# Kernel tuning notes

Measured on AMD Instinct MI355X. Metric: run time of the kernel, lower is better.

Reference implementation:

```python
import jax, jax.numpy as jnp
import numpy as np

D_MODEL = 1024
N_HEADS = 16
N_KV_HEADS = 4
HEAD_DIM = 64


def setup_inputs() -> dict:
    key = jax.random.key(0)
    ks = jax.random.split(key, 5)
    B, T, P = 2, 512, 8
    scale = 1.0 / np.sqrt(D_MODEL)
    return {
        "hidden_states": jax.random.normal(ks[0], (B, T, P, D_MODEL), dtype=jnp.float32),
        # weights stored [in, out] so y = x @ W (same math as nn.Linear with W^T)
        "Wq": jax.random.normal(ks[1], (D_MODEL, N_HEADS * HEAD_DIM), dtype=jnp.float32) * scale,
        "Wk": jax.random.normal(ks[2], (D_MODEL, N_KV_HEADS * HEAD_DIM), dtype=jnp.float32) * scale,
        "Wv": jax.random.normal(ks[3], (D_MODEL, N_KV_HEADS * HEAD_DIM), dtype=jnp.float32) * scale,
        "Wo": jax.random.normal(ks[4], (N_HEADS * HEAD_DIM, D_MODEL), dtype=jnp.float32) * scale,
    }


def _rope_tables(T, d):
    half = d // 2
    inv_freq = 1.0 / (10000.0 ** (jnp.arange(half, dtype=jnp.float32) / half))
    pos = jnp.arange(T, dtype=jnp.float32)
    angles = pos[:, None] * inv_freq[None, :]  # (T, half)
    return jnp.cos(angles), jnp.sin(angles)


def _apply_rope(x, cos, sin):
    # x: (B, P, T, H, d); cos/sin: (T, d/2)
    half = x.shape[-1] // 2
    x1, x2 = x[..., :half], x[..., half:]
    c = cos[None, None, :, None, :]
    s = sin[None, None, :, None, :]
    return jnp.concatenate([x1 * c - x2 * s, x1 * s + x2 * c], axis=-1)


def reference(hidden_states, Wq, Wk, Wv, Wo):
    B, T, P, _ = hidden_states.shape
    x = jnp.transpose(hidden_states, (0, 2, 1, 3))  # (B, P, T, C)
    q = (x @ Wq).reshape(B, P, T, N_HEADS, HEAD_DIM)
    k = (x @ Wk).reshape(B, P, T, N_KV_HEADS, HEAD_DIM)
    v = (x @ Wv).reshape(B, P, T, N_KV_HEADS, HEAD_DIM)

    rep = N_HEADS // N_KV_HEADS
    k = jnp.repeat(k, rep, axis=3)  # (B,P,T,H,d) interleaved like torch repeat/view
    v = jnp.repeat(v, rep, axis=3)

    cos, sin = _rope_tables(T, HEAD_DIM)
    q = _apply_rope(q, cos, sin)
    k = _apply_rope(k, cos, sin)

    # (B,P,H,T,d)
    q = jnp.transpose(q, (0, 1, 3, 2, 4))
    k = jnp.transpose(k, (0, 1, 3, 2, 4))
    v = jnp.transpose(v, (0, 1, 3, 2, 4))

    attn = jnp.einsum("bphqd,bphkd->bphqk", q, k) / jnp.sqrt(
        jnp.asarray(HEAD_DIM, q.dtype))
    attn = jax.nn.softmax(attn, axis=-1)
    out = jnp.einsum("bphqk,bphkd->bphqd", attn, v)
    out = jnp.transpose(out, (0, 1, 3, 2, 4)).reshape(B, P, T, N_HEADS * HEAD_DIM)
    out = jnp.transpose(out, (0, 2, 1, 3))  # (B, T, P, H*d)
    return out @ Wo
```

## Files before the change

### kernel.cpp

```cpp
#include <hip/hip_runtime.h>
#include <stdint.h>


typedef __attribute__((ext_vector_type(8))) short bf16x8;
typedef __attribute__((ext_vector_type(4))) float f32x4;
typedef __attribute__((ext_vector_type(16))) float f32x16;
typedef __attribute__((ext_vector_type(4))) unsigned short us4;
typedef __attribute__((ext_vector_type(8))) unsigned short us8;

static __device__ __forceinline__ unsigned short f2bf(float f) {
  unsigned u = __float_as_uint(f);
  u += 0x7fffu + ((u >> 16) & 1u);
  return (unsigned short)(u >> 16);
}

static __device__ __forceinline__ void ld_lds16(const void* g, void* l) {
  __builtin_amdgcn_global_load_lds(
      (const __attribute__((address_space(1))) void*)g,
      (__attribute__((address_space(3))) void*)l, 16, 0, 0);
}

static __device__ __forceinline__ f32x4 mfma16(bf16x8 a, bf16x8 b, f32x4 c) {
  return __builtin_amdgcn_mfma_f32_16x16x32_bf16(a, b, c, 0, 0, 0);
}
static __device__ __forceinline__ f32x16 mfma32(bf16x8 a, bf16x8 b, f32x16 c) {
  return __builtin_amdgcn_mfma_f32_32x32x16_bf16(a, b, c, 0, 0, 0);
}

__global__ __launch_bounds__(256) void conv_all(
    const float* __restrict__ hs, const float* __restrict__ Wq,
    const float* __restrict__ Wk, const float* __restrict__ Wv,
    const float* __restrict__ Wo, unsigned short* __restrict__ xb,
    unsigned short* __restrict__ wqkv, unsigned short* __restrict__ wot) {
  __shared__ float tile[64][65];
  int bid = blockIdx.x, tid = threadIdx.x;
  if (bid < 8192) {
    int gid = bid * 256 + tid;
    size_t e = (size_t)gid * 4;
    int r = (int)(e >> 10);
    int d = (int)(e & 1023);
    int b = r >> 12, p = (r >> 9) & 7, t = r & 511;
    const float4* src = (const float4*)(hs + ((((size_t)b * 512 + t) * 8 + p) << 10) + d);
    float4 v = *src;
    us4 o;
    o.x = f2bf(v.x); o.y = f2bf(v.y); o.z = f2bf(v.z); o.w = f2bf(v.w);
    *(us4*)(xb + e) = o;
    return;
  }
  int tb = bid - 8192;
  const float* W; unsigned short* Wt; int N, tc0, tn0;
  if (tb < 256)      { W = Wq; Wt = wqkv;                       N = 1024; tc0 = (tb >> 4) * 64;          tn0 = (tb & 15) * 64; }
  else if (tb < 320) { W = Wk; Wt = wqkv + (size_t)1024 * 1024; N = 256;  tc0 = ((tb - 256) >> 2) * 64;  tn0 = ((tb - 256) & 3) * 64; }
  else if (tb < 384) { W = Wv; Wt = wqkv + (size_t)1280 * 1024; N = 256;  tc0 = ((tb - 320) >> 2) * 64;  tn0 = ((tb - 320) & 3) * 64; }
  else               { W = Wo; Wt = wot;                        N = 1024; tc0 = ((tb - 384) >> 4) * 64;  tn0 = ((tb - 384) & 15) * 64; }
  int tr = tid >> 4, tc = tid & 15;
#pragma unroll
  for (int i = 0; i < 4; ++i) {
    int c = tr + i * 16;
    float4 v = *(const float4*)(W + (size_t)(tc0 + c) * N + tn0 + tc * 4);
    tile[c][tc * 4 + 0] = v.x; tile[c][tc * 4 + 1] = v.y;
    tile[c][tc * 4 + 2] = v.z; tile[c][tc * 4 + 3] = v.w;
  }
  __syncthreads();
#pragma unroll
  for (int i = 0; i < 4; ++i) {
    int n = tr + i * 16;
    us4 o;
    o.x = f2bf(tile[tc * 4 + 0][n]); o.y = f2bf(tile[tc * 4 + 1][n]);
    o.z = f2bf(tile[tc * 4 + 2][n]); o.w = f2bf(tile[tc * 4 + 3][n]);
    *(us4*)(Wt + (size_t)(tn0 + n) * 1024 + tc0 + tc * 4) = o;
  }
}

__global__ __launch_bounds__(512, 2) void gemm_qkv(
    const unsigned short* __restrict__ A, const unsigned short* __restrict__ Bt,
    unsigned short* __restrict__ qb, unsigned short* __restrict__ kb,
    unsigned short* __restrict__ vtb) {
  constexpr int K = 1024;
  constexpr int KT = K / 64;
  __shared__ __align__(16) unsigned short Sm[2][2][256 * 64];
  unsigned short* Cs = &Sm[0][0][0];

  int tid = threadIdx.x;
  int lane = tid & 63, wid = tid >> 6;
  int quad = lane >> 4, lo = lane & 15;
  int wg = (blockIdx.x & 7) * 24 + (blockIdx.x >> 3);
  int tn = wg % 6, tm = wg / 6;
  int wr = wid >> 2, wc = wid & 3;
  int srow = lane >> 3, schunk = lane & 7;
  int cg = schunk ^ srow;

  const unsigned short* pa = A + ((size_t)(tm * 256) + wid * 8 + srow) * K + cg * 8;
  const unsigned short* pb = Bt + ((size_t)(tn * 256) + wid * 8 + srow) * K + cg * 8;

  f32x4 z = {0.f, 0.f, 0.f, 0.f};
  f32x4 acc[8][4];
#pragma unroll
  for (int i = 0; i < 8; ++i)
#pragma unroll
    for (int j = 0; j < 4; ++j) acc[i][j] = z;

  auto stage = [&](int t, int p) {
#pragma unroll
    for (int i = 0; i < 4; ++i) {
      ld_lds16(pa + (size_t)i * 64 * K + t * 64,
               (char*)&Sm[p][0][0] + (wid * 8 + i * 64) * 128);
      ld_lds16(pb + (size_t)i * 64 * K + t * 64,
               (char*)&Sm[p][1][0] + (wid * 8 + i * 64) * 128);
    }
  };

  stage(0, 0);
  stage(1, 1);
  asm volatile("s_waitcnt vmcnt(8)" ::: "memory");
  asm volatile("s_barrier" ::: "memory");

  bf16x8 af[4][2], bb0[2][2], bb1[2][2];

  for (int t = 0; t < KT; ++t) {
    int p = t & 1;
    const unsigned short* As = &Sm[p][0][0];
    const unsigned short* Bs = &Sm[p][1][0];

#pragma unroll
    for (int mi = 0; mi < 4; ++mi)
#pragma unroll
      for (int kx = 0; kx < 2; ++kx) {
        int row = wr * 128 + mi * 16 + lo;
        int cgx = (quad + kx * 4) ^ (row & 7);
        af[mi][kx] = *(const bf16x8*)(As + (size_t)row * 64 + cgx * 8);
      }
#pragma unroll
    for (int ni = 0; ni < 2; ++ni)
#pragma unroll
      for (int kx = 0; kx < 2; ++kx) {
        int row = wc * 64 + ni * 16 + lo;
        int cgx = (quad + kx * 4) ^ (row & 7);
        bb0[ni][kx] = *(const bf16x8*)(Bs + (size_t)row * 64 + cgx * 8);
      }
    asm volatile("s_barrier" ::: "memory");
    __builtin_amdgcn_s_setprio(1);
#pragma unroll
    for (int kx = 0; kx < 2; ++kx)
#pragma unroll
      for (int mi = 0; mi < 4; ++mi)
#pragma unroll
        for (int ni = 0; ni < 2; ++ni)
          acc[mi][ni] = mfma16(af[mi][kx], bb0[ni][kx], acc[mi][ni]);
    __builtin_amdgcn_s_setprio(0);
    asm volatile("s_barrier" ::: "memory");

#pragma unroll
    for (int ni = 0; ni < 2; ++ni)
#pragma unroll
      for (int kx = 0; kx < 2; ++kx) {
        int row = wc * 64 + (ni + 2) * 16 + lo;
        int cgx = (quad + kx * 4) ^ (row & 7);
        bb1[ni][kx] = *(const bf16x8*)(Bs + (size_t)row * 64 + cgx * 8);
      }
    asm volatile("s_barrier" ::: "memory");
    __builtin_amdgcn_s_setprio(1);
#pragma unroll
    for (int kx = 0; kx < 2; ++kx)
#pragma unroll
      for (int mi = 0; mi < 4; ++mi)
#pragma unroll
        for (int ni = 0; ni < 2; ++ni)
          acc[mi][ni + 2] = mfma16(af[mi][kx], bb1[ni][kx], acc[mi][ni + 2]);
    __builtin_amdgcn_s_setprio(0);
    asm volatile("s_barrier" ::: "memory");

#pragma unroll
    for (int mi = 0; mi < 4; ++mi)
#pragma unroll
      for (int kx = 0; kx < 2; ++kx) {
        int row = wr * 128 + 64 + mi * 16 + lo;
        int cgx = (quad + kx * 4) ^ (row & 7);
        af[mi][kx] = *(const bf16x8*)(As + (size_t)row * 64 + cgx * 8);
      }
    asm volatile("s_barrier" ::: "memory");
    __builtin_amdgcn_s_setprio(1);
#pragma unroll
    for (int kx = 0; kx < 2; ++kx)
#pragma unroll
      for (int mi = 0; mi < 4; ++mi)
#pragma unroll
        for (int ni = 0; ni < 2; ++ni)
          acc[mi + 4][ni + 2] = mfma16(af[mi][kx], bb1[ni][kx], acc[mi + 4][ni + 2]);
    __builtin_amdgcn_s_setprio(0);
    asm volatile("s_barrier" ::: "memory");

    bool pf = (t + 2 < KT);
    if (pf) stage(t + 2, p);
    __builtin_amdgcn_s_setprio(1);
#pragma unroll
    for (int kx = 0; kx < 2; ++kx)
#pragma unroll
      for (int mi = 0; mi < 4; ++mi)
#pragma unroll
        for (int ni = 0; ni < 2; ++ni)
          acc[mi + 4][ni] = mfma16(af[mi][kx], bb0[ni][kx], acc[mi + 4][ni]);
    __builtin_amdgcn_s_setprio(0);
    if (pf) asm volatile("s_waitcnt vmcnt(8)" ::: "memory");
    else    asm volatile("s_waitcnt vmcnt(0)" ::: "memory");
    asm volatile("s_barrier" ::: "memory");
  }

  if (tn < 5) {
    float qscale = (tn < 4) ? 0.125f : 1.0f;
#pragma unroll
    for (int mi = 0; mi < 8; ++mi)
#pragma unroll
      for (int r = 0; r < 4; ++r) {
        int row = wr * 128 + mi * 16 + quad * 4 + r;
        int tpos = (tm * 256 + row) & 511;
#pragma unroll
        for (int ni = 0; ni < 2; ++ni) {
          float invf = exp2f((float)(ni * 16 + lo) * -0.41524101186092029f);
          float ang = (float)tpos * invf;
          float s, c;
          __sincosf(ang, &s, &c);
          float x1 = acc[mi][ni][r], x2 = acc[mi][ni + 2][r];
          acc[mi][ni][r]     = (x1 * c - x2 * s) * qscale;
          acc[mi][ni + 2][r] = (x1 * s + x2 * c) * qscale;
        }
      }
#pragma unroll
    for (int mi = 0; mi < 8; ++mi)
#pragma unroll
      for (int ni = 0; ni < 4; ++ni)
#pragma unroll
        for (int r = 0; r < 4; ++r) {
          int row = wr * 128 + mi * 16 + quad * 4 + r;
          int col = wc * 64 + ni * 16 + lo;
          int cs = col ^ (((row >> 2) & 3) << 3);
          Cs[row * 256 + cs] = f2bf(acc[mi][ni][r]);
        }
    __syncthreads();
    int tc = tid & 31, ro = tid >> 5;
#pragma unroll
    for (int it = 0; it < 16; ++it) {
      int row = ro + 16 * it;
      int cs = (tc * 8) ^ (((row >> 2) & 3) << 3);
      us8 v = *(const us8*)(Cs + row * 256 + cs);
      size_t grow = (size_t)(tm * 256 + row);
      if (tn < 4) *(us8*)(qb + grow * 1024 + tn * 256 + tc * 8) = v;
      else        *(us8*)(kb + grow * 256 + tc * 8) = v;
    }
  } else {
#pragma unroll
    for (int mi = 0; mi < 8; ++mi)
#pragma unroll
      for (int ni = 0; ni < 4; ++ni)
#pragma unroll
        for (int r = 0; r < 4; ++r) {
          int trow = wr * 128 + mi * 16 + quad * 4 + r;
          int col = wc * 64 + ni * 16 + lo;
          Cs[col * 256 + (trow ^ ((col & 7) << 3))] = f2bf(acc[mi][ni][r]);
        }
    __syncthreads();
    int t0 = (tid & 31) * 8, colIdx = tid >> 5;
    int bp = tm >> 1, tbase = (tm & 1) * 256;
#pragma unroll
    for (int it = 0; it < 16; ++it) {
      int col = colIdx + it * 16;
      us8 v = *(const us8*)(Cs + col * 256 + (t0 ^ ((col & 7) << 3)));
      int hh = col >> 6, dd = col & 63;
      *(us8*)(vtb + (((size_t)(bp * 4 + hh)) * 64 + dd) * 512 + tbase + t0) = v;
    }
  }
}

__global__ __launch_bounds__(512, 2) void gemm_o(
    const unsigned short* __restrict__ A, const unsigned short* __restrict__ Bt,
    float* __restrict__ out) {
  constexpr int K = 1024;
  constexpr int KT = K / 64;
  __shared__ __align__(16) unsigned short Sm[2][(128 + 256) * 64];

  int tid = threadIdx.x;
  int lane = tid & 63, wid = tid >> 6;
  int quad = lane >> 4, lo = lane & 15;
  int wg = (blockIdx.x & 7) * 32 + (blockIdx.x >> 3);
  int tn = wg & 3, tm = wg >> 2;
  int wr = wid >> 2, wc = wid & 3;
  int srow = lane >> 3, schunk = lane & 7;
  int cg = schunk ^ srow;

  const unsigned short* pa = A + ((size_t)(tm * 128) + wid * 8 + srow) * K + cg * 8;
  const unsigned short* pb = Bt + ((size_t)(tn * 256) + wid * 8 + srow) * K + cg * 8;

  f32x4 z = {0.f, 0.f, 0.f, 0.f};
  f32x4 acc[4][4];
#pragma unroll
  for (int i = 0; i < 4; ++i)
#pragma unroll
    for (int j = 0; j < 4; ++j) acc[i][j] = z;

  auto stage = [&](int t, int p) {
    unsigned short* As = &Sm[p][0];
    unsigned short* Bs = &Sm[p][128 * 64];
#pragma unroll
    for (int i = 0; i < 2; ++i)
      ld_lds16(pa + (size_t)i * 64 * K + t * 64,
               (char*)As + (wid * 8 + i * 64) * 128);
#pragma unroll
    for (int i = 0; i < 4; ++i)
      ld_lds16(pb + (size_t)i * 64 * K + t * 64,
               (char*)Bs + (wid * 8 + i * 64) * 128);
  };

  stage(0, 0);
  stage(1, 1);
  asm volatile("s_waitcnt vmcnt(6)" ::: "memory");
  asm volatile("s_barrier" ::: "memory");

  bf16x8 af[4][2], bb0[2][2], bb1[2][2];

  for (int t = 0; t < KT; ++t) {
    int p = t & 1;
    const unsigned short* As = &Sm[p][0];
    const unsigned short* Bs = &Sm[p][128 * 64];

#pragma unroll
    for (int mi = 0; mi < 4; ++mi)
#pragma unroll
      for (int kx = 0; kx < 2; ++kx) {
        int row = wr * 64 + mi * 16 + lo;
        int cgx = (quad + kx * 4) ^ (row & 7);
        af[mi][kx] = *(const bf16x8*)(As + (size_t)row * 64 + cgx * 8);
      }
#pragma unroll
    for (int ni = 0; ni < 2; ++ni)
#pragma unroll
      for (int kx = 0; kx < 2; ++kx) {
        int row = wc * 64 + ni * 16 + lo;
        int cgx = (quad + kx * 4) ^ (row & 7);
        bb0[ni][kx] = *(const bf16x8*)(Bs + (size_t)row * 64 + cgx * 8);
      }
    asm volatile("s_barrier" ::: "memory");
    __builtin_amdgcn_s_setprio(1);
#pragma unroll
    for (int kx = 0; kx < 2; ++kx)
#pragma unroll
      for (int mi = 0; mi < 4; ++mi)
#pragma unroll
        for (int ni = 0; ni < 2; ++ni)
          acc[mi][ni] = mfma16(af[mi][kx], bb0[ni][kx], acc[mi][ni]);
    __builtin_amdgcn_s_setprio(0);
    asm volatile("s_barrier" ::: "memory");

#pragma unroll
    for (int ni = 0; ni < 2; ++ni)
#pragma unroll
      for (int kx = 0; kx < 2; ++kx) {
        int row = wc * 64 + (ni + 2) * 16 + lo;
        int cgx = (quad + kx * 4) ^ (row & 7);
        bb1[ni][kx] = *(const bf16x8*)(Bs + (size_t)row * 64 + cgx * 8);
      }
    asm volatile("s_barrier" ::: "memory");
    __builtin_amdgcn_s_setprio(1);
#pragma unroll
    for (int kx = 0; kx < 2; ++kx)
#pragma unroll
      for (int mi = 0; mi < 4; ++mi)
#pragma unroll
        for (int ni = 0; ni < 2; ++ni)
          acc[mi][ni + 2] = mfma16(af[mi][kx], bb1[ni][kx], acc[mi][ni + 2]);
    __builtin_amdgcn_s_setprio(0);
    asm volatile("s_barrier" ::: "memory");

    bool pf = (t + 2 < KT);
    if (pf) {
      stage(t + 2, p);
      asm volatile("s_waitcnt vmcnt(6)" ::: "memory");
    } else {
      asm volatile("s_waitcnt vmcnt(0)" ::: "memory");
    }
    asm volatile("s_barrier" ::: "memory");
  }

#pragma unroll
  for (int mi = 0; mi < 4; ++mi) {
    for (int ni = 0; ni < 4; ++ni) {
      int col = tn * 256 + wc * 64 + ni * 16 + lo;
      for (int r = 0; r < 4; ++r) {
        int grow = tm * 128 + wr * 64 + mi * 16 + quad * 4 + r;
        int bp = grow >> 9, tt = grow & 511;
        int b = bp >> 3, pp = bp & 7;
        out[((((size_t)b * 512 + tt) * 8 + pp) << 10) + col] = acc[mi][ni][r];
      }
    }
  }
}

__global__ __launch_bounds__(512, 4) void attn(
    const unsigned short* __restrict__ qb, const unsigned short* __restrict__ kb,
    const unsigned short* __restrict__ vtb, unsigned short* __restrict__ ao) {
  __shared__ __align__(16) unsigned short Qs[256 * 64];
  __shared__ __align__(16) unsigned short Ks[2][64 * 64];
  __shared__ __align__(16) unsigned short Vs[2][64 * 64];

  int tid = threadIdx.x;
  int lane = tid & 63, wid = tid >> 6;
  int lo32 = lane & 31, hl = lane >> 5;
  int wg = (blockIdx.x & 7) * 64 + (blockIdx.x >> 3);
  int qt = wg & 1, bph = wg >> 1;
  int head = bph & 15, bp = bph >> 4;
  int kvh = head >> 2;
  int t0 = qt * 256;
  int srow = lane >> 3, schunk = lane & 7;

  const unsigned short* qg = qb + ((size_t)(bp * 512 + t0)) * 1024 + head * 64;
  const unsigned short* kg = kb + ((size_t)bp * 512) * 256 + kvh * 64;
  const unsigned short* vg = vtb + ((size_t)(bp * 4 + kvh)) * 64 * 512;

#pragma unroll
  for (int i = 0; i < 4; ++i) {
    int row = wid * 8 + i * 64 + srow;
    int cg = schunk ^ (row & 7);
    ld_lds16(qg + (size_t)row * 1024 + cg * 8, (char*)Qs + (wid * 8 + i * 64) * 128);
  }

  auto stageKV = [&](int kt, int p) {
    int row = wid * 8 + srow;
    int cg = schunk ^ (row & 7);
    ld_lds16(kg + (size_t)(kt * 64 + row) * 256 + cg * 8, (char*)&Ks[p][0] + (wid * 8) * 128);
    ld_lds16(vg + (size_t)row * 512 + kt * 64 + cg * 8, (char*)&Vs[p][0] + (wid * 8) * 128);
  };

  stageKV(0, 0);
  stageKV(1, 1);
  asm volatile("s_waitcnt vmcnt(2)" ::: "memory");
  asm volatile("s_barrier" ::: "memory");

  f32x16 z16 = {0.f};
  f32x16 o0 = z16, o1 = z16;
  float psum = 0.f;
  int qrow = wid * 32 + lo32;

  for (int kt = 0; kt < 8; ++kt) {
    int p = kt & 1;
    const unsigned short* Kp = &Ks[p][0];
    const unsigned short* Vp = &Vs[p][0];

    f32x16 st0 = z16, st1 = z16;
#pragma unroll
    for (int kkc = 0; kkc < 4; ++kkc) {
      int ch = 2 * kkc + hl;
      bf16x8 qf = *(const bf16x8*)(Qs + (size_t)qrow * 64 + ((ch ^ (qrow & 7)) * 8));
      bf16x8 kf0 = *(const bf16x8*)(Kp + (size_t)lo32 * 64 + ((ch ^ (lo32 & 7)) * 8));
      bf16x8 kf1 = *(const bf16x8*)(Kp + (size_t)(32 + lo32) * 64 + ((ch ^ (lo32 & 7)) * 8));
      st0 = mfma32(kf0, qf, st0);
      st1 = mfma32(kf1, qf, st1);
    }

#pragma unroll
    for (int t = 0; t < 2; ++t) {
      const f32x16& stv = t ? st1 : st0;
      unsigned pk[8], xpk[8];
#pragma unroll
      for (int pp = 0; pp < 8; ++pp) {
        float e0 = __expf(stv[2 * pp]);
        float e1 = __expf(stv[2 * pp + 1]);
        psum += e0 + e1;
        pk[pp] = ((__float_as_uint(e0) + 0x8000u) >> 16) |
                 ((__float_as_uint(e1) + 0x8000u) & 0xffff0000u);
      }
#pragma unroll
      for (int pp = 0; pp < 8; ++pp) xpk[pp] = (unsigned)__shfl_xor((int)pk[pp], 32);
#pragma unroll
      for (int cc = 0; cc < 2; ++cc) {
        int o = cc * 4;
        union { unsigned u[4]; bf16x8 v; } af;
        if (hl == 0) {
          af.u[0] = pk[o];      af.u[1] = pk[o + 1];
          af.u[2] = xpk[o];     af.u[3] = xpk[o + 1];
        } else {
          af.u[0] = xpk[o + 2]; af.u[1] = xpk[o + 3];
          af.u[2] = pk[o + 2];  af.u[3] = pk[o + 3];
        }
        int vch = 2 * (t * 2 + cc) + hl;
        bf16x8 v0 = *(const bf16x8*)(Vp + (size_t)lo32 * 64 + ((vch ^ (lo32 & 7)) * 8));
        bf16x8 v1 = *(const bf16x8*)(Vp + (size_t)(32 + lo32) * 64 + ((vch ^ (lo32 & 7)) * 8));
        o0 = mfma32(af.v, v0, o0);
        o1 = mfma32(af.v, v1, o1);
      }
    }

    if (kt == 7) break;
    asm volatile("s_barrier" ::: "memory");
    if (kt < 6) {
      stageKV(kt + 2, p);
      asm volatile("s_waitcnt vmcnt(2)" ::: "memory");
    } else {
      asm volatile("s_waitcnt vmcnt(0)" ::: "memory");
    }
    asm volatile("s_barrier" ::: "memory");
  }

  psum += __shfl_xor(psum, 32);
  float inv = 1.f / psum;
#pragma unroll
  for (int r = 0; r < 16; ++r) {
    int q_r = (r & 3) + 8 * (r >> 2) + 4 * hl;
    float sc = __shfl(inv, q_r);
    size_t grow = (size_t)(bp * 512 + t0 + wid * 32 + q_r);
    ao[grow * 1024 + head * 64 + lo32]      = f2bf(o0[r] * sc);
    ao[grow * 1024 + head * 64 + 32 + lo32] = f2bf(o1[r] * sc);
  }
}

extern "C" void kernel_launch(void* const* d_in, const int* in_sizes, int n_in,
                              void* d_out, int out_size, void* d_ws, size_t ws_size,
                              hipStream_t stream) {
  const float* hs = (const float*)d_in[0];
  const float* Wq = (const float*)d_in[1];
  const float* Wk = (const float*)d_in[2];
  const float* Wv = (const float*)d_in[3];
  const float* Wo = (const float*)d_in[4];
  float* out = (float*)d_out;

  unsigned short* xb   = (unsigned short*)d_ws;
  unsigned short* wqkv = xb + (size_t)8192 * 1024;
  unsigned short* wot  = wqkv + (size_t)1536 * 1024;
  unsigned short* qbuf = wot + (size_t)1024 * 1024;
  unsigned short* kbuf = qbuf + (size_t)8192 * 1024;
  unsigned short* vtb  = kbuf + (size_t)8192 * 256;
  unsigned short* ao   = xb;

  conv_all<<<8832, 256, 0, stream>>>(hs, Wq, Wk, Wv, Wo, xb, wqkv, wot);
  gemm_qkv<<<192, 512, 0, stream>>>(xb, wqkv, qbuf, kbuf, vtb);
  attn<<<512, 512, 0, stream>>>(qbuf, kbuf, vtb, ao);
  gemm_o<<<256, 512, 0, stream>>>(ao, wot, out);
}
```

Baseline: 181.9 us.

## Fuse all four stages into one persistent cooperative kernel with grid syncs

Replaces the four separate launches (convert, QKV GEMM, attention, output GEMM) with a single cooperative kernel of 256 blocks that runs each stage in turn, separated by grid-wide syncs. The goal is to remove per-launch overhead and the gaps between kernels. The cost is that every stage is now limited to 256 blocks of 512 threads with a shared LDS budget. Stages that used to launch many more blocks (the conversion pass and attention) must loop, and the grid barriers add their own cost.

```diff
diff --git a/kernel.cpp b/kernel.cpp
--- a/kernel.cpp
+++ b/kernel.cpp
@@ -1,5 +1,8 @@
 #include <hip/hip_runtime.h>
+#include <hip/hip_cooperative_groups.h>
 #include <stdint.h>
+
+namespace cg = cooperative_groups;
 
 
 typedef __attribute__((ext_vector_type(8))) short bf16x8;
@@ -27,487 +30,507 @@
   return __builtin_amdgcn_mfma_f32_32x32x16_bf16(a, b, c, 0, 0, 0);
 }
 
-__global__ __launch_bounds__(256) void conv_all(
+__global__ __launch_bounds__(512, 2) void mega(
     const float* __restrict__ hs, const float* __restrict__ Wq,
     const float* __restrict__ Wk, const float* __restrict__ Wv,
-    const float* __restrict__ Wo, unsigned short* __restrict__ xb,
-    unsigned short* __restrict__ wqkv, unsigned short* __restrict__ wot) {
-  __shared__ float tile[64][65];
+    const float* __restrict__ Wo,
+    unsigned short* __restrict__ xb, unsigned short* __restrict__ wqkv,
+    unsigned short* __restrict__ wot, unsigned short* __restrict__ qb,
+    unsigned short* __restrict__ kb, unsigned short* __restrict__ vtb,
+    float* __restrict__ out) {
+  __shared__ __align__(16) unsigned char LDSb[131072];
+  cg::grid_group grid = cg::this_grid();
   int bid = blockIdx.x, tid = threadIdx.x;
-  if (bid < 8192) {
-    int gid = bid * 256 + tid;
-    size_t e = (size_t)gid * 4;
-    int r = (int)(e >> 10);
-    int d = (int)(e & 1023);
-    int b = r >> 12, p = (r >> 9) & 7, t = r & 511;
-    const float4* src = (const float4*)(hs + ((((size_t)b * 512 + t) * 8 + p) << 10) + d);
-    float4 v = *src;
-    us4 o;
-    o.x = f2bf(v.x); o.y = f2bf(v.y); o.z = f2bf(v.z); o.w = f2bf(v.w);
-    *(us4*)(xb + e) = o;
-    return;
+
+  {
+    float (*tile)[65] = (float(*)[65])LDSb;
+    for (int i = 0; i < 3; ++i) {
+      int tb = i * 256 + bid;
+      bool act = (tb < 640) && (tid < 256);
+      const float* W = nullptr; unsigned short* Wt = nullptr;
+      int N = 0, tc0 = 0, tn0 = 0;
+      if (act) {
+        if (tb < 256)      { W = Wq; Wt = wqkv;                       N = 1024; tc0 = (tb >> 4) * 64;          tn0 = (tb & 15) * 64; }
+        else if (tb < 320) { W = Wk; Wt = wqkv + (size_t)1024 * 1024; N = 256;  tc0 = ((tb - 256) >> 2) * 64;  tn0 = ((tb - 256) & 3) * 64; }
+        else if (tb < 384) { W = Wv; Wt = wqkv + (size_t)1280 * 1024; N = 256;  tc0 = ((tb - 320) >> 2) * 64;  tn0 = ((tb - 320) & 3) * 64; }
+        else               { W = Wo; Wt = wot;                        N = 1024; tc0 = ((tb - 384) >> 4) * 64;  tn0 = ((tb - 384) & 15) * 64; }
+      }
+      int tr = tid >> 4, tc = tid & 15;
+      if (act) {
+#pragma unroll
+        for (int k = 0; k < 4; ++k) {
+          int c = tr + k * 16;
+          float4 v = *(const float4*)(W + (size_t)(tc0 + c) * N + tn0 + tc * 4);
+          tile[c][tc * 4 + 0] = v.x; tile[c][tc * 4 + 1] = v.y;
+          tile[c][tc * 4 + 2] = v.z; tile[c][tc * 4 + 3] = v.w;
+        }
+      }
+      __syncthreads();
+      if (act) {
+#pragma unroll
+        for (int k = 0; k < 4; ++k) {
+          int n = tr + k * 16;
+          us4 o;
+          o.x = f2bf(tile[tc * 4 + 0][n]); o.y = f2bf(tile[tc * 4 + 1][n]);
+          o.z = f2bf(tile[tc * 4 + 2][n]); o.w = f2bf(tile[tc * 4 + 3][n]);
+          *(us4*)(Wt + (size_t)(tn0 + n) * 1024 + tc0 + tc * 4) = o;
+        }
+      }
+      __syncthreads();
+    }
+    for (int it = 0; it < 16; ++it) {
+      int gid = it * 131072 + bid * 512 + tid;
+      size_t e = (size_t)gid * 4;
+      int r = (int)(e >> 10);
+      int d = (int)(e & 1023);
+      int b = r >> 12, p = (r >> 9) & 7, t = r & 511;
+      const float4* src = (const float4*)(hs + ((((size_t)b * 512 + t) * 8 + p) << 10) + d);
+      float4 v = *src;
+      us4 o;
+      o.x = f2bf(v.x); o.y = f2bf(v.y); o.z = f2bf(v.z); o.w = f2bf(v.w);
+      *(us4*)(xb + e) = o;
+    }
   }
-  int tb = bid - 8192;
-  const float* W; unsigned short* Wt; int N, tc0, tn0;
-  if (tb < 256)      { W = Wq; Wt = wqkv;                       N = 1024; tc0 = (tb >> 4) * 64;          tn0 = (tb & 15) * 64; }
-  else if (tb < 320) { W = Wk; Wt = wqkv + (size_t)1024 * 1024; N = 256;  tc0 = ((tb - 256) >> 2) * 64;  tn0 = ((tb - 256) & 3) * 64; }
-  else if (tb < 384) { W = Wv; Wt = wqkv + (size_t)1280 * 1024; N = 256;  tc0 = ((tb - 320) >> 2) * 64;  tn0 = ((tb - 320) & 3) * 64; }
-  else               { W = Wo; Wt = wot;                        N = 1024; tc0 = ((tb - 384) >> 4) * 64;  tn0 = ((tb - 384) & 15) * 64; }
-  int tr = tid >> 4, tc = tid & 15;
-#pragma unroll
-  for (int i = 0; i < 4; ++i) {
-    int c = tr + i * 16;
-    float4 v = *(const float4*)(W + (size_t)(tc0 + c) * N + tn0 + tc * 4);
-    tile[c][tc * 4 + 0] = v.x; tile[c][tc * 4 + 1] = v.y;
-    tile[c][tc * 4 + 2] = v.z; tile[c][tc * 4 + 3] = v.w;
-  }
-  __syncthreads();
-#pragma unroll
-  for (int i = 0; i < 4; ++i) {
-    int n = tr + i * 16;
-    us4 o;
-    o.x = f2bf(tile[tc * 4 + 0][n]); o.y = f2bf(tile[tc * 4 + 1][n]);
-    o.z = f2bf(tile[tc * 4 + 2][n]); o.w = f2bf(tile[tc * 4 + 3][n]);
-    *(us4*)(Wt + (size_t)(tn0 + n) * 1024 + tc0 + tc * 4) = o;
-  }
-}
-
-__global__ __launch_bounds__(512, 2) void gemm_qkv(
-    const unsigned short* __restrict__ A, const unsigned short* __restrict__ Bt,
-    unsigned short* __restrict__ qb, unsigned short* __restrict__ kb,
-    unsigned short* __restrict__ vtb) {
-  constexpr int K = 1024;
-  constexpr int KT = K / 64;
-  __shared__ __align__(16) unsigned short Sm[2][2][256 * 64];
-  unsigned short* Cs = &Sm[0][0][0];
-
-  int tid = threadIdx.x;
-  int lane = tid & 63, wid = tid >> 6;
-  int quad = lane >> 4, lo = lane & 15;
-  int wg = (blockIdx.x & 7) * 24 + (blockIdx.x >> 3);
-  int tn = wg % 6, tm = wg / 6;
-  int wr = wid >> 2, wc = wid & 3;
-  int srow = lane >> 3, schunk = lane & 7;
-  int cg = schunk ^ srow;
-
-  const unsigned short* pa = A + ((size_t)(tm * 256) + wid * 8 + srow) * K + cg * 8;
-  const unsigned short* pb = Bt + ((size_t)(tn * 256) + wid * 8 + srow) * K + cg * 8;
-
-  f32x4 z = {0.f, 0.f, 0.f, 0.f};
-  f32x4 acc[8][4];
-#pragma unroll
-  for (int i = 0; i < 8; ++i)
-#pragma unroll
-    for (int j = 0; j < 4; ++j) acc[i][j] = z;
-
-  auto stage = [&](int t, int p) {
-#pragma unroll
-    for (int i = 0; i < 4; ++i) {
-      ld_lds16(pa + (size_t)i * 64 * K + t * 64,
-               (char*)&Sm[p][0][0] + (wid * 8 + i * 64) * 128);
-      ld_lds16(pb + (size_t)i * 64 * K + t * 64,
-               (char*)&Sm[p][1][0] + (wid * 8 + i * 64) * 128);
-    }
-  };
-
-  stage(0, 0);
-  stage(1, 1);
-  asm volatile("s_waitcnt vmcnt(8)" ::: "memory");
-  asm volatile("s_barrier" ::: "memory");
-
-  bf16x8 af[4][2], bb0[2][2], bb1[2][2];
-
-  for (int t = 0; t < KT; ++t) {
-    int p = t & 1;
-    const unsigned short* As = &Sm[p][0][0];
-    const unsigned short* Bs = &Sm[p][1][0];
-
-#pragma unroll
-    for (int mi = 0; mi < 4; ++mi)
-#pragma unroll
-      for (int kx = 0; kx < 2; ++kx) {
-        int row = wr * 128 + mi * 16 + lo;
-        int cgx = (quad + kx * 4) ^ (row & 7);
-        af[mi][kx] = *(const bf16x8*)(As + (size_t)row * 64 + cgx * 8);
-      }
-#pragma unroll
-    for (int ni = 0; ni < 2; ++ni)
-#pragma unroll
-      for (int kx = 0; kx < 2; ++kx) {
-        int row = wc * 64 + ni * 16 + lo;
-        int cgx = (quad + kx * 4) ^ (row & 7);
-        bb0[ni][kx] = *(const bf16x8*)(Bs + (size_t)row * 64 + cgx * 8);
-      }
+  grid.sync();
+
+  if (bid < 192) {
+    constexpr int K = 1024;
+    constexpr int KT = K / 64;
+    unsigned short* SmB = (unsigned short*)LDSb;
+    unsigned short* Cs = SmB;
+
+    int lane = tid & 63, wid = tid >> 6;
+    int quad = lane >> 4, lo = lane & 15;
+    int wg = (bid & 7) * 24 + (bid >> 3);
+    int tn = wg % 6, tm = wg / 6;
+    int wr = wid >> 2, wc = wid & 3;
+    int srow = lane >> 3, schunk = lane & 7;
+    int cg_ = schunk ^ srow;
+
+    const unsigned short* pa = xb + ((size_t)(tm * 256) + wid * 8 + srow) * K + cg_ * 8;
+    const unsigned short* pb = wqkv + ((size_t)(tn * 256) + wid * 8 + srow) * K + cg_ * 8;
+
+    f32x4 z = {0.f, 0.f, 0.f, 0.f};
+    f32x4 acc[8][4];
+#pragma unroll
+    for (int i = 0; i < 8; ++i)
+#pragma unroll
+      for (int j = 0; j < 4; ++j) acc[i][j] = z;
+
+    auto stage = [&](int t, int p) {
+#pragma unroll
+      for (int i = 0; i < 4; ++i) {
+        ld_lds16(pa + (size_t)i * 64 * K + t * 64,
+                 (char*)(SmB + (size_t)p * 2 * 16384) + (wid * 8 + i * 64) * 128);
+        ld_lds16(pb + (size_t)i * 64 * K + t * 64,
+                 (char*)(SmB + (size_t)(p * 2 + 1) * 16384) + (wid * 8 + i * 64) * 128);
+      }
+    };
+
+    stage(0, 0);
+    stage(1, 1);
+    asm volatile("s_waitcnt vmcnt(8)" ::: "memory");
     asm volatile("s_barrier" ::: "memory");
-    __builtin_amdgcn_s_setprio(1);
-#pragma unroll
-    for (int kx = 0; kx < 2; ++kx)
+
+    bf16x8 af[4][2], bb0[2][2], bb1[2][2];
+
+    for (int t = 0; t < KT; ++t) {
+      int p = t & 1;
+      const unsigned short* As = SmB + (size_t)p * 2 * 16384;
+      const unsigned short* Bs = SmB + (size_t)(p * 2 + 1) * 16384;
+
 #pragma unroll
       for (int mi = 0; mi < 4; ++mi)
 #pragma unroll
-        for (int ni = 0; ni < 2; ++ni)
-          acc[mi][ni] = mfma16(af[mi][kx], bb0[ni][kx], acc[mi][ni]);
-    __builtin_amdgcn_s_setprio(0);
-    asm volatile("s_barrier" ::: "memory");
-
-#pragma unroll
-    for (int ni = 0; ni < 2; ++ni)
-#pragma unroll
-      for (int kx = 0; kx < 2; ++kx) {
-        int row = wc * 64 + (ni + 2) * 16 + lo;
-        int cgx = (quad + kx * 4) ^ (row & 7);
-        bb1[ni][kx] = *(const bf16x8*)(Bs + (size_t)row * 64 + cgx * 8);
-      }
-    asm volatile("s_barrier" ::: "memory");
-    __builtin_amdgcn_s_setprio(1);
-#pragma unroll
-    for (int kx = 0; kx < 2; ++kx)
+        for (int kx = 0; kx < 2; ++kx) {
+          int row = wr * 128 + mi * 16 + lo;
+          int cgx = (quad + kx * 4) ^ (row & 7);
+          af[mi][kx] = *(const bf16x8*)(As + (size_t)row * 64 + cgx * 8);
+        }
+#pragma unroll
+      for (int ni = 0; ni < 2; ++ni)
+#pragma unroll
+        for (int kx = 0; kx < 2; ++kx) {
+          int row = wc * 64 + ni * 16 + lo;
+          int cgx = (quad + kx * 4) ^ (row & 7);
+          bb0[ni][kx] = *(const bf16x8*)(Bs + (size_t)row * 64 + cgx * 8);
+        }
+      asm volatile("s_barrier" ::: "memory");
+      __builtin_amdgcn_s_setprio(1);
+#pragma unroll
+      for (int kx = 0; kx < 2; ++kx)
+#pragma unroll
+        for (int mi = 0; mi < 4; ++mi)
+#pragma unroll
+          for (int ni = 0; ni < 2; ++ni)
+            acc[mi][ni] = mfma16(af[mi][kx], bb0[ni][kx], acc[mi][ni]);
+      __builtin_amdgcn_s_setprio(0);
+      asm volatile("s_barrier" ::: "memory");
+
+#pragma unroll
+      for (int ni = 0; ni < 2; ++ni)
+#pragma unroll
+        for (int kx = 0; kx < 2; ++kx) {
+          int row = wc * 64 + (ni + 2) * 16 + lo;
+          int cgx = (quad + kx * 4) ^ (row & 7);
+          bb1[ni][kx] = *(const bf16x8*)(Bs + (size_t)row * 64 + cgx * 8);
+        }
+      asm volatile("s_barrier" ::: "memory");
+      __builtin_amdgcn_s_setprio(1);
+#pragma unroll
+      for (int kx = 0; kx < 2; ++kx)
+#pragma unroll
+        for (int mi = 0; mi < 4; ++mi)
+#pragma unroll
+          for (int ni = 0; ni < 2; ++ni)
+            acc[mi][ni + 2] = mfma16(af[mi][kx], bb1[ni][kx], acc[mi][ni + 2]);
+      __builtin_amdgcn_s_setprio(0);
+      asm volatile("s_barrier" ::: "memory");
+
 #pragma unroll
       for (int mi = 0; mi < 4; ++mi)
 #pragma unroll
-        for (int ni = 0; ni < 2; ++ni)
-          acc[mi][ni + 2] = mfma16(af[mi][kx], bb1[ni][kx], acc[mi][ni + 2]);
-    __builtin_amdgcn_s_setprio(0);
-    asm volatile("s_barrier" ::: "memory");
-
-#pragma unroll
-    for (int mi = 0; mi < 4; ++mi)
-#pragma unroll
-      for (int kx = 0; kx < 2; ++kx) {
-        int row = wr * 128 + 64 + mi * 16 + lo;
-        int cgx = (quad + kx * 4) ^ (row & 7);
-        af[mi][kx] = *(const bf16x8*)(As + (size_t)row * 64 + cgx * 8);
-      }
-    asm volatile("s_barrier" ::: "memory");
-    __builtin_amdgcn_s_setprio(1);
-#pragma unroll
-    for (int kx = 0; kx < 2; ++kx)
-#pragma unroll
-      for (int mi = 0; mi < 4; ++mi)
-#pragma unroll
-        for (int ni = 0; ni < 2; ++ni)
-          acc[mi + 4][ni + 2] = mfma16(af[mi][kx], bb1[ni][kx], acc[mi + 4][ni + 2]);
-    __builtin_amdgcn_s_setprio(0);
-    asm volatile("s_barrier" ::: "memory");
-
-    bool pf = (t + 2 < KT);
-    if (pf) stage(t + 2, p);
-    __builtin_amdgcn_s_setprio(1);
-#pragma unroll
-    for (int kx = 0; kx < 2; ++kx)
-#pragma unroll
-      for (int mi = 0; mi < 4; ++mi)
-#pragma unroll
-        for (int ni = 0; ni < 2; ++ni)
-          acc[mi + 4][ni] = mfma16(af[mi][kx], bb0[ni][kx], acc[mi + 4][ni]);
-    __builtin_amdgcn_s_setprio(0);
-    if (pf) asm volatile("s_waitcnt vmcnt(8)" ::: "memory");
-    else    asm volatile("s_waitcnt vmcnt(0)" ::: "memory");
-    asm volatile("s_barrier" ::: "memory");
-  }
-
-  if (tn < 5) {
-    float qscale = (tn < 4) ? 0.125f : 1.0f;
-#pragma unroll
-    for (int mi = 0; mi < 8; ++mi)
-#pragma unroll
-      for (int r = 0; r < 4; ++r) {
-        int row = wr * 128 + mi * 16 + quad * 4 + r;
-        int tpos = (tm * 256 + row) & 511;
-#pragma unroll
-        for (int ni = 0; ni < 2; ++ni) {
-          float invf = exp2f((float)(ni * 16 + lo) * -0.41524101186092029f);
-          float ang = (float)tpos * invf;
-          float s, c;
-          __sincosf(ang, &s, &c);
-          float x1 = acc[mi][ni][r], x2 = acc[mi][ni + 2][r];
-          acc[mi][ni][r]     = (x1 * c - x2 * s) * qscale;
-          acc[mi][ni + 2][r] = (x1 * s + x2 * c) * qscale;
-        }
-      }
-#pragma unroll
-    for (int mi = 0; mi < 8; ++mi)
-#pragma unroll
-      for (int ni = 0; ni < 4; ++ni)
+        for (int kx = 0; kx < 2; ++kx) {
+          int row = wr * 128 + 64 + mi * 16 + lo;
+          int cgx = (quad + kx * 4) ^ (row & 7);
+          af[mi][kx] = *(const bf16x8*)(As + (size_t)row * 64 + cgx * 8);
+        }
+      asm volatile("s_barrier" ::: "memory");
+      __builtin_amdgcn_s_setprio(1);
+#pragma unroll
+      for (int kx = 0; kx < 2; ++kx)
+#pragma unroll
+        for (int mi = 0; mi < 4; ++mi)
+#pragma unroll
+          for (int ni = 0; ni < 2; ++ni)
+            acc[mi + 4][ni + 2] = mfma16(af[mi][kx], bb1[ni][kx], acc[mi + 4][ni + 2]);
+      __builtin_amdgcn_s_setprio(0);
+      asm volatile("s_barrier" ::: "memory");
+
+      bool pf = (t + 2 < KT);
+      if (pf) stage(t + 2, p);
+      __builtin_amdgcn_s_setprio(1);
+#pragma unroll
+      for (int kx = 0; kx < 2; ++kx)
+#pragma unroll
+        for (int mi = 0; mi < 4; ++mi)
+#pragma unroll
+          for (int ni = 0; ni < 2; ++ni)
+            acc[mi + 4][ni] = mfma16(af[mi][kx], bb0[ni][kx], acc[mi + 4][ni]);
+      __builtin_amdgcn_s_setprio(0);
+      if (pf) asm volatile("s_waitcnt vmcnt(8)" ::: "memory");
+      else    asm volatile("s_waitcnt vmcnt(0)" ::: "memory");
+      asm volatile("s_barrier" ::: "memory");
+    }
+
+    __syncthreads();
+
+    if (tn < 5) {
+      float qscale = (tn < 4) ? 0.125f : 1.0f;
+#pragma unroll
+      for (int mi = 0; mi < 8; ++mi)
 #pragma unroll
         for (int r = 0; r < 4; ++r) {
           int row = wr * 128 + mi * 16 + quad * 4 + r;
-          int col = wc * 64 + ni * 16 + lo;
-          int cs = col ^ (((row >> 2) & 3) << 3);
-          Cs[row * 256 + cs] = f2bf(acc[mi][ni][r]);
-        }
-    __syncthreads();
-    int tc = tid & 31, ro = tid >> 5;
-#pragma unroll
-    for (int it = 0; it < 16; ++it) {
-      int row = ro + 16 * it;
-      int cs = (tc * 8) ^ (((row >> 2) & 3) << 3);
-      us8 v = *(const us8*)(Cs + row * 256 + cs);
-      size_t grow = (size_t)(tm * 256 + row);
-      if (tn < 4) *(us8*)(qb + grow * 1024 + tn * 256 + tc * 8) = v;
-      else        *(us8*)(kb + grow * 256 + tc * 8) = v;
-    }
-  } else {
-#pragma unroll
-    for (int mi = 0; mi < 8; ++mi)
-#pragma unroll
-      for (int ni = 0; ni < 4; ++ni)
-#pragma unroll
+          int tpos = (tm * 256 + row) & 511;
+#pragma unroll
+          for (int ni = 0; ni < 2; ++ni) {
+            float invf = exp2f((float)(ni * 16 + lo) * -0.41524101186092029f);
+            float ang = (float)tpos * invf;
+            float s, c;
+            __sincosf(ang, &s, &c);
+            float x1 = acc[mi][ni][r], x2 = acc[mi][ni + 2][r];
+            acc[mi][ni][r]     = (x1 * c - x2 * s) * qscale;
+            acc[mi][ni + 2][r] = (x1 * s + x2 * c) * qscale;
+          }
+        }
+#pragma unroll
+      for (int mi = 0; mi < 8; ++mi)
+#pragma unroll
+        for (int ni = 0; ni < 4; ++ni)
+#pragma unroll
+          for (int r = 0; r < 4; ++r) {
+            int row = wr * 128 + mi * 16 + quad * 4 + r;
+            int col = wc * 64 + ni * 16 + lo;
+            int cs = col ^ (((row >> 2) & 3) << 3);
+            Cs[row * 256 + cs] = f2bf(acc[mi][ni][r]);
+          }
+      __syncthreads();
+      int tc = tid & 31, ro = tid >> 5;
+#pragma unroll
+      for (int it = 0; it < 16; ++it) {
+        int row = ro + 16 * it;
+        int cs = (tc * 8) ^ (((row >> 2) & 3) << 3);
+        us8 v = *(const us8*)(Cs + row * 256 + cs);
+        size_t grow = (size_t)(tm * 256 + row);
+        if (tn < 4) *(us8*)(qb + grow * 1024 + tn * 256 + tc * 8) = v;
+        else        *(us8*)(kb + grow * 256 + tc * 8) = v;
+      }
+    } else {
+#pragma unroll
+      for (int mi = 0; mi < 8; ++mi)
+#pragma unroll
+        for (int ni = 0; ni < 4; ++ni)
+#pragma unroll
+          for (int r = 0; r < 4; ++r) {
+            int trow = wr * 128 + mi * 16 + quad * 4 + r;
+            int col = wc * 64 + ni * 16 + lo;
+            Cs[col * 256 + (trow ^ ((col & 7) << 3))] = f2bf(acc[mi][ni][r]);
+          }
+      __syncthreads();
+      int t0 = (tid & 31) * 8, colIdx = tid >> 5;
+      int bp = tm >> 1, tbase = (tm & 1) * 256;
+#pragma unroll
+      for (int it = 0; it < 16; ++it) {
+        int col = colIdx + it * 16;
+        us8 v = *(const us8*)(Cs + col * 256 + (t0 ^ ((col & 7) << 3)));
+        int hh = col >> 6, dd = col & 63;
+        *(us8*)(vtb + (((size_t)(bp * 4 + hh)) * 64 + dd) * 512 + tbase + t0) = v;
+      }
+    }
+  }
+  grid.sync();
+
+  {
+    unsigned short* Qs = (unsigned short*)LDSb;
+    unsigned short* KsB = Qs + 256 * 64;
+    unsigned short* VsB = KsB + 2 * 64 * 64;
+    unsigned short* ao = xb;
+
+    int lane = tid & 63, wid = tid >> 6;
+    int lo32 = lane & 31, hl = lane >> 5;
+    int srow = lane >> 3, schunk = lane & 7;
+
+    for (int u = 0; u < 2; ++u) {
+      __syncthreads();
+      int uu = bid + u * 256;
+      int wg = (uu & 7) * 64 + (uu >> 3);
+      int qt = wg & 1, bph = wg >> 1;
+      int head = bph & 15, bp = bph >> 4;
+      int kvh = head >> 2;
+      int t0 = qt * 256;
+
+      const unsigned short* qg = qb + ((size_t)(bp * 512 + t0)) * 1024 + head * 64;
+      const unsigned short* kg = kb + ((size_t)bp * 512) * 256 + kvh * 64;
+      const unsigned short* vg = vtb + ((size_t)(bp * 4 + kvh)) * 64 * 512;
+
+#pragma unroll
+      for (int i = 0; i < 4; ++i) {
+        int row = wid * 8 + i * 64 + srow;
+        int cg_ = schunk ^ (row & 7);
+        ld_lds16(qg + (size_t)row * 1024 + cg_ * 8, (char*)Qs + (wid * 8 + i * 64) * 128);
+      }
+
+      auto stageKV = [&](int kt, int p) {
+        int row = wid * 8 + srow;
+        int cg_ = schunk ^ (row & 7);
+        ld_lds16(kg + (size_t)(kt * 64 + row) * 256 + cg_ * 8, (char*)(KsB + p * 4096) + (wid * 8) * 128);
+        ld_lds16(vg + (size_t)row * 512 + kt * 64 + cg_ * 8, (char*)(VsB + p * 4096) + (wid * 8) * 128);
+      };
+
+      stageKV(0, 0);
+      stageKV(1, 1);
+      asm volatile("s_waitcnt vmcnt(2)" ::: "memory");
+      asm volatile("s_barrier" ::: "memory");
+
+      f32x16 z16 = {0.f};
+      f32x16 o0 = z16, o1 = z16;
+      float psum = 0.f;
+      int qrow = wid * 32 + lo32;
+
+      for (int kt = 0; kt < 8; ++kt) {
+        int p = kt & 1;
+        const unsigned short* Kp = KsB + p * 4096;
+        const unsigned short* Vp = VsB + p * 4096;
+
+        f32x16 st0 = z16, st1 = z16;
+#pragma unroll
+        for (int kkc = 0; kkc < 4; ++kkc) {
+          int ch = 2 * kkc + hl;
+          bf16x8 qf = *(const bf16x8*)(Qs + (size_t)qrow * 64 + ((ch ^ (qrow & 7)) * 8));
+          bf16x8 kf0 = *(const bf16x8*)(Kp + (size_t)lo32 * 64 + ((ch ^ (lo32 & 7)) * 8));
+          bf16x8 kf1 = *(const bf16x8*)(Kp + (size_t)(32 + lo32) * 64 + ((ch ^ (lo32 & 7)) * 8));
+          st0 = mfma32(kf0, qf, st0);
+          st1 = mfma32(kf1, qf, st1);
+        }
+
+#pragma unroll
+        for (int t = 0; t < 2; ++t) {
+          const f32x16& stv = t ? st1 : st0;
+          unsigned pk[8], xpk[8];
+#pragma unroll
+          for (int pp = 0; pp < 8; ++pp) {
+            float e0 = __expf(stv[2 * pp]);
+            float e1 = __expf(stv[2 * pp + 1]);
+            psum += e0 + e1;
+            pk[pp] = ((__float_as_uint(e0) + 0x8000u) >> 16) |
+                     ((__float_as_uint(e1) + 0x8000u) & 0xffff0000u);
+          }
+#pragma unroll
+          for (int pp = 0; pp < 8; ++pp) xpk[pp] = (unsigned)__shfl_xor((int)pk[pp], 32);
+#pragma unroll
+          for (int cc = 0; cc < 2; ++cc) {
+            int o = cc * 4;
+            union { unsigned u[4]; bf16x8 v; } afr;
+            if (hl == 0) {
+              afr.u[0] = pk[o];      afr.u[1] = pk[o + 1];
+              afr.u[2] = xpk[o];     afr.u[3] = xpk[o + 1];
+            } else {
+              afr.u[0] = xpk[o + 2]; afr.u[1] = xpk[o + 3];
+              afr.u[2] = pk[o + 2];  afr.u[3] = pk[o + 3];
+            }
+            int vch = 2 * (t * 2 + cc) + hl;
+            bf16x8 v0 = *(const bf16x8*)(Vp + (size_t)lo32 * 64 + ((vch ^ (lo32 & 7)) * 8));
+            bf16x8 v1 = *(const bf16x8*)(Vp + (size_t)(32 + lo32) * 64 + ((vch ^ (lo32 & 7)) * 8));
+            o0 = mfma32(afr.v, v0, o0);
+            o1 = mfma32(afr.v, v1, o1);
+          }
+        }
+
+        if (kt == 7) break;
+        asm volatile("s_barrier" ::: "memory");
+        if (kt < 6) {
+          stageKV(kt + 2, p);
+          asm volatile("s_waitcnt vmcnt(2)" ::: "memory");
+        } else {
+          asm volatile("s_waitcnt vmcnt(0)" ::: "memory");
+        }
+        asm volatile("s_barrier" ::: "memory");
+      }
+
+      psum += __shfl_xor(psum, 32);
+      float inv = 1.f / psum;
+#pragma unroll
+      for (int r = 0; r < 16; ++r) {
+        int q_r = (r & 3) + 8 * (r >> 2) + 4 * hl;
+        float sc = __shfl(inv, q_r);
+        size_t grow = (size_t)(bp * 512 + t0 + wid * 32 + q_r);
+        ao[grow * 1024 + head * 64 + lo32]      = f2bf(o0[r] * sc);
+        ao[grow * 1024 + head * 64 + 32 + lo32] = f2bf(o1[r] * sc);
+      }
+    }
+  }
+  grid.sync();
+
+  {
+    constexpr int K = 1024;
+    constexpr int KT = K / 64;
+    unsigned short* SmD = (unsigned short*)LDSb;
+    const unsigned short* Ain = xb;
+
+    int lane = tid & 63, wid = tid >> 6;
+    int quad = lane >> 4, lo = lane & 15;
+    int wg = (bid & 7) * 32 + (bid >> 3);
+    int tn = wg & 3, tm = wg >> 2;
+    int wr = wid >> 2, wc = wid & 3;
+    int srow = lane >> 3, schunk = lane & 7;
+    int cg_ = schunk ^ srow;
+
+    const unsigned short* pa = Ain + ((size_t)(tm * 128) + wid * 8 + srow) * K + cg_ * 8;
+    const unsigned short* pb = wot + ((size_t)(tn * 256) + wid * 8 + srow) * K + cg_ * 8;
+
+    f32x4 z = {0.f, 0.f, 0.f, 0.f};
+    f32x4 acc[4][4];
+#pragma unroll
+    for (int i = 0; i < 4; ++i)
+#pragma unroll
+      for (int j = 0; j < 4; ++j) acc[i][j] = z;
+
+    auto stage = [&](int t, int p) {
+      unsigned short* As = SmD + (size_t)p * 24576;
+      unsigned short* Bs = As + 128 * 64;
+#pragma unroll
+      for (int i = 0; i < 2; ++i)
+        ld_lds16(pa + (size_t)i * 64 * K + t * 64,
+                 (char*)As + (wid * 8 + i * 64) * 128);
+#pragma unroll
+      for (int i = 0; i < 4; ++i)
+        ld_lds16(pb + (size_t)i * 64 * K + t * 64,
+                 (char*)Bs + (wid * 8 + i * 64) * 128);
+    };
+
+    stage(0, 0);
+    stage(1, 1);
+    asm volatile("s_waitcnt vmcnt(6)" ::: "memory");
+    asm volatile("s_barrier" ::: "memory");
+
+    bf16x8 af[4][2], bb0[2][2], bb1[2][2];
+
+    for (int t = 0; t < KT; ++t) {
+      int p = t & 1;
+      const unsigned short* As = SmD + (size_t)p * 24576;
+      const unsigned short* Bs = As + 128 * 64;
+
+#pragma unroll
+      for (int mi = 0; mi < 4; ++mi)
+#pragma unroll
+        for (int kx = 0; kx < 2; ++kx) {
+          int row = wr * 64 + mi * 16 + lo;
+          int cgx = (quad + kx * 4) ^ (row & 7);
+          af[mi][kx] = *(const bf16x8*)(As + (size_t)row * 64 + cgx * 8);
+        }
+#pragma unroll
+      for (int ni = 0; ni < 2; ++ni)
+#pragma unroll
+        for (int kx = 0; kx < 2; ++kx) {
+          int row = wc * 64 + ni * 16 + lo;
+          int cgx = (quad + kx * 4) ^ (row & 7);
+          bb0[ni][kx] = *(const bf16x8*)(Bs + (size_t)row * 64 + cgx * 8);
+        }
+      asm volatile("s_barrier" ::: "memory");
+      __builtin_amdgcn_s_setprio(1);
+#pragma unroll
+      for (int kx = 0; kx < 2; ++kx)
+#pragma unroll
+        for (int mi = 0; mi < 4; ++mi)
+#pragma unroll
+          for (int ni = 0; ni < 2; ++ni)
+            acc[mi][ni] = mfma16(af[mi][kx], bb0[ni][kx], acc[mi][ni]);
+      __builtin_amdgcn_s_setprio(0);
+      asm volatile("s_barrier" ::: "memory");
+
+#pragma unroll
+      for (int ni = 0; ni < 2; ++ni)
+#pragma unroll
+        for (int kx = 0; kx < 2; ++kx) {
+          int row = wc * 64 + (ni + 2) * 16 + lo;
+          int cgx = (quad + kx * 4) ^ (row & 7);
+          bb1[ni][kx] = *(const bf16x8*)(Bs + (size_t)row * 64 + cgx * 8);
+        }
+      asm volatile("s_barrier" ::: "memory");
+      __builtin_amdgcn_s_setprio(1);
+#pragma unroll
+      for (int kx = 0; kx < 2; ++kx)
+#pragma unroll
+        for (int mi = 0; mi < 4; ++mi)
+#pragma unroll
+          for (int ni = 0; ni < 2; ++ni)
+            acc[mi][ni + 2] = mfma16(af[mi][kx], bb1[ni][kx], acc[mi][ni + 2]);
+      __builtin_amdgcn_s_setprio(0);
+      asm volatile("s_barrier" ::: "memory");
+
+      bool pf = (t + 2 < KT);
+      if (pf) {
+        stage(t + 2, p);
+        asm volatile("s_waitcnt vmcnt(6)" ::: "memory");
+      } else {
+        asm volatile("s_waitcnt vmcnt(0)" ::: "memory");
+      }
+      asm volatile("s_barrier" ::: "memory");
+    }
+
+#pragma unroll
+    for (int mi = 0; mi < 4; ++mi) {
+      for (int ni = 0; ni < 4; ++ni) {
+        int col = tn * 256 + wc * 64 + ni * 16 + lo;
         for (int r = 0; r < 4; ++r) {
-          int trow = wr * 128 + mi * 16 + quad * 4 + r;
-          int col = wc * 64 + ni * 16 + lo;
-          Cs[col * 256 + (trow ^ ((col & 7) << 3))] = f2bf(acc[mi][ni][r]);
-        }
-    __syncthreads();
-    int t0 = (tid & 31) * 8, colIdx = tid >> 5;
-    int bp = tm >> 1, tbase = (tm & 1) * 256;
-#pragma unroll
-    for (int it = 0; it < 16; ++it) {
-      int col = colIdx + it * 16;
-      us8 v = *(const us8*)(Cs + col * 256 + (t0 ^ ((col & 7) << 3)));
-      int hh = col >> 6, dd = col & 63;
-      *(us8*)(vtb + (((size_t)(bp * 4 + hh)) * 64 + dd) * 512 + tbase + t0) = v;
-    }
-  }
-}
-
-__global__ __launch_bounds__(512, 2) void gemm_o(
-    const unsigned short* __restrict__ A, const unsigned short* __restrict__ Bt,
-    float* __restrict__ out) {
-  constexpr int K = 1024;
-  constexpr int KT = K / 64;
-  __shared__ __align__(16) unsigned short Sm[2][(128 + 256) * 64];
-
-  int tid = threadIdx.x;
-  int lane = tid & 63, wid = tid >> 6;
-  int quad = lane >> 4, lo = lane & 15;
-  int wg = (blockIdx.x & 7) * 32 + (blockIdx.x >> 3);
-  int tn = wg & 3, tm = wg >> 2;
-  int wr = wid >> 2, wc = wid & 3;
-  int srow = lane >> 3, schunk = lane & 7;
-  int cg = schunk ^ srow;
-
-  const unsigned short* pa = A + ((size_t)(tm * 128) + wid * 8 + srow) * K + cg * 8;
-  const unsigned short* pb = Bt + ((size_t)(tn * 256) + wid * 8 + srow) * K + cg * 8;
-
-  f32x4 z = {0.f, 0.f, 0.f, 0.f};
-  f32x4 acc[4][4];
-#pragma unroll
-  for (int i = 0; i < 4; ++i)
-#pragma unroll
-    for (int j = 0; j < 4; ++j) acc[i][j] = z;
-
-  auto stage = [&](int t, int p) {
-    unsigned short* As = &Sm[p][0];
-    unsigned short* Bs = &Sm[p][128 * 64];
-#pragma unroll
-    for (int i = 0; i < 2; ++i)
-      ld_lds16(pa + (size_t)i * 64 * K + t * 64,
-               (char*)As + (wid * 8 + i * 64) * 128);
-#pragma unroll
-    for (int i = 0; i < 4; ++i)
-      ld_lds16(pb + (size_t)i * 64 * K + t * 64,
-               (char*)Bs + (wid * 8 + i * 64) * 128);
-  };
-
-  stage(0, 0);
-  stage(1, 1);
-  asm volatile("s_waitcnt vmcnt(6)" ::: "memory");
-  asm volatile("s_barrier" ::: "memory");
-
-  bf16x8 af[4][2], bb0[2][2], bb1[2][2];
-
-  for (int t = 0; t < KT; ++t) {
-    int p = t & 1;
-    const unsigned short* As = &Sm[p][0];
-    const unsigned short* Bs = &Sm[p][128 * 64];
-
-#pragma unroll
-    for (int mi = 0; mi < 4; ++mi)
-#pragma unroll
-      for (int kx = 0; kx < 2; ++kx) {
-        int row = wr * 64 + mi * 16 + lo;
-        int cgx = (quad + kx * 4) ^ (row & 7);
-        af[mi][kx] = *(const bf16x8*)(As + (size_t)row * 64 + cgx * 8);
-      }
-#pragma unroll
-    for (int ni = 0; ni < 2; ++ni)
-#pragma unroll
-      for (int kx = 0; kx < 2; ++kx) {
-        int row = wc * 64 + ni * 16 + lo;
-        int cgx = (quad + kx * 4) ^ (row & 7);
-        bb0[ni][kx] = *(const bf16x8*)(Bs + (size_t)row * 64 + cgx * 8);
-      }
-    asm volatile("s_barrier" ::: "memory");
-    __builtin_amdgcn_s_setprio(1);
-#pragma unroll
-    for (int kx = 0; kx < 2; ++kx)
-#pragma unroll
-      for (int mi = 0; mi < 4; ++mi)
-#pragma unroll
-        for (int ni = 0; ni < 2; ++ni)
-          acc[mi][ni] = mfma16(af[mi][kx], bb0[ni][kx], acc[mi][ni]);
-    __builtin_amdgcn_s_setprio(0);
-    asm volatile("s_barrier" ::: "memory");
-
-#pragma unroll
-    for (int ni = 0; ni < 2; ++ni)
-#pragma unroll
-      for (int kx = 0; kx < 2; ++kx) {
-        int row = wc * 64 + (ni + 2) * 16 + lo;
-        int cgx = (quad + kx * 4) ^ (row & 7);
-        bb1[ni][kx] = *(const bf16x8*)(Bs + (size_t)row * 64 + cgx * 8);
-      }
-    asm volatile("s_barrier" ::: "memory");
-    __builtin_amdgcn_s_setprio(1);
-#pragma unroll
-    for (int kx = 0; kx < 2; ++kx)
-#pragma unroll
-      for (int mi = 0; mi < 4; ++mi)
-#pragma unroll
-        for (int ni = 0; ni < 2; ++ni)
-          acc[mi][ni + 2] = mfma16(af[mi][kx], bb1[ni][kx], acc[mi][ni + 2]);
-    __builtin_amdgcn_s_setprio(0);
-    asm volatile("s_barrier" ::: "memory");
-
-    bool pf = (t + 2 < KT);
-    if (pf) {
-      stage(t + 2, p);
-      asm volatile("s_waitcnt vmcnt(6)" ::: "memory");
-    } else {
-      asm volatile("s_waitcnt vmcnt(0)" ::: "memory");
-    }
-    asm volatile("s_barrier" ::: "memory");
-  }
-
-#pragma unroll
-  for (int mi = 0; mi < 4; ++mi) {
-    for (int ni = 0; ni < 4; ++ni) {
-      int col = tn * 256 + wc * 64 + ni * 16 + lo;
-      for (int r = 0; r < 4; ++r) {
-        int grow = tm * 128 + wr * 64 + mi * 16 + quad * 4 + r;
-        int bp = grow >> 9, tt = grow & 511;
-        int b = bp >> 3, pp = bp & 7;
-        out[((((size_t)b * 512 + tt) * 8 + pp) << 10) + col] = acc[mi][ni][r];
-      }
-    }
-  }
-}
-
-__global__ __launch_bounds__(512, 4) void attn(
-    const unsigned short* __restrict__ qb, const unsigned short* __restrict__ kb,
-    const unsigned short* __restrict__ vtb, unsigned short* __restrict__ ao) {
-  __shared__ __align__(16) unsigned short Qs[256 * 64];
-  __shared__ __align__(16) unsigned short Ks[2][64 * 64];
-  __shared__ __align__(16) unsigned short Vs[2][64 * 64];
-
-  int tid = threadIdx.x;
-  int lane = tid & 63, wid = tid >> 6;
-  int lo32 = lane & 31, hl = lane >> 5;
-  int wg = (blockIdx.x & 7) * 64 + (blockIdx.x >> 3);
-  int qt = wg & 1, bph = wg >> 1;
-  int head = bph & 15, bp = bph >> 4;
-  int kvh = head >> 2;
-  int t0 = qt * 256;
-  int srow = lane >> 3, schunk = lane & 7;
-
-  const unsigned short* qg = qb + ((size_t)(bp * 512 + t0)) * 1024 + head * 64;
-  const unsigned short* kg = kb + ((size_t)bp * 512) * 256 + kvh * 64;
-  const unsigned short* vg = vtb + ((size_t)(bp * 4 + kvh)) * 64 * 512;
-
-#pragma unroll
-  for (int i = 0; i < 4; ++i) {
-    int row = wid * 8 + i * 64 + srow;
-    int cg = schunk ^ (row & 7);
-    ld_lds16(qg + (size_t)row * 1024 + cg * 8, (char*)Qs + (wid * 8 + i * 64) * 128);
-  }
-
-  auto stageKV = [&](int kt, int p) {
-    int row = wid * 8 + srow;
-    int cg = schunk ^ (row & 7);
-    ld_lds16(kg + (size_t)(kt * 64 + row) * 256 + cg * 8, (char*)&Ks[p][0] + (wid * 8) * 128);
-    ld_lds16(vg + (size_t)row * 512 + kt * 64 + cg * 8, (char*)&Vs[p][0] + (wid * 8) * 128);
-  };
-
-  stageKV(0, 0);
-  stageKV(1, 1);
-  asm volatile("s_waitcnt vmcnt(2)" ::: "memory");
-  asm volatile("s_barrier" ::: "memory");
-
-  f32x16 z16 = {0.f};
-  f32x16 o0 = z16, o1 = z16;
-  float psum = 0.f;
-  int qrow = wid * 32 + lo32;
-
-  for (int kt = 0; kt < 8; ++kt) {
-    int p = kt & 1;
-    const unsigned short* Kp = &Ks[p][0];
-    const unsigned short* Vp = &Vs[p][0];
-
-    f32x16 st0 = z16, st1 = z16;
-#pragma unroll
-    for (int kkc = 0; kkc < 4; ++kkc) {
-      int ch = 2 * kkc + hl;
-      bf16x8 qf = *(const bf16x8*)(Qs + (size_t)qrow * 64 + ((ch ^ (qrow & 7)) * 8));
-      bf16x8 kf0 = *(const bf16x8*)(Kp + (size_t)lo32 * 64 + ((ch ^ (lo32 & 7)) * 8));
-      bf16x8 kf1 = *(const bf16x8*)(Kp + (size_t)(32 + lo32) * 64 + ((ch ^ (lo32 & 7)) * 8));
-      st0 = mfma32(kf0, qf, st0);
-      st1 = mfma32(kf1, qf, st1);
-    }
-
-#pragma unroll
-    for (int t = 0; t < 2; ++t) {
-      const f32x16& stv = t ? st1 : st0;
-      unsigned pk[8], xpk[8];
-#pragma unroll
-      for (int pp = 0; pp < 8; ++pp) {
-        float e0 = __expf(stv[2 * pp]);
-        float e1 = __expf(stv[2 * pp + 1]);
-        psum += e0 + e1;
-        pk[pp] = ((__float_as_uint(e0) + 0x8000u) >> 16) |
-                 ((__float_as_uint(e1) + 0x8000u) & 0xffff0000u);
-      }
-#pragma unroll
-      for (int pp = 0; pp < 8; ++pp) xpk[pp] = (unsigned)__shfl_xor((int)pk[pp], 32);
-#pragma unroll
-      for (int cc = 0; cc < 2; ++cc) {
-        int o = cc * 4;
-        union { unsigned u[4]; bf16x8 v; } af;
-        if (hl == 0) {
-          af.u[0] = pk[o];      af.u[1] = pk[o + 1];
-          af.u[2] = xpk[o];     af.u[3] = xpk[o + 1];
-        } else {
-          af.u[0] = xpk[o + 2]; af.u[1] = xpk[o + 3];
-          af.u[2] = pk[o + 2];  af.u[3] = pk[o + 3];
-        }
-        int vch = 2 * (t * 2 + cc) + hl;
-        bf16x8 v0 = *(const bf16x8*)(Vp + (size_t)lo32 * 64 + ((vch ^ (lo32 & 7)) * 8));
-        bf16x8 v1 = *(const bf16x8*)(Vp + (size_t)(32 + lo32) * 64 + ((vch ^ (lo32 & 7)) * 8));
-        o0 = mfma32(af.v, v0, o0);
-        o1 = mfma32(af.v, v1, o1);
-      }
-    }
-
-    if (kt == 7) break;
-    asm volatile("s_barrier" ::: "memory");
-    if (kt < 6) {
-      stageKV(kt + 2, p);
-      asm volatile("s_waitcnt vmcnt(2)" ::: "memory");
-    } else {
-      asm volatile("s_waitcnt vmcnt(0)" ::: "memory");
-    }
-    asm volatile("s_barrier" ::: "memory");
-  }
-
-  psum += __shfl_xor(psum, 32);
-  float inv = 1.f / psum;
-#pragma unroll
-  for (int r = 0; r < 16; ++r) {
-    int q_r = (r & 3) + 8 * (r >> 2) + 4 * hl;
-    float sc = __shfl(inv, q_r);
-    size_t grow = (size_t)(bp * 512 + t0 + wid * 32 + q_r);
-    ao[grow * 1024 + head * 64 + lo32]      = f2bf(o0[r] * sc);
-    ao[grow * 1024 + head * 64 + 32 + lo32] = f2bf(o1[r] * sc);
+          int grow = tm * 128 + wr * 64 + mi * 16 + quad * 4 + r;
+          int bp = grow >> 9, tt = grow & 511;
+          int b = bp >> 3, pp = bp & 7;
+          out[((((size_t)b * 512 + tt) * 8 + pp) << 10) + col] = acc[mi][ni][r];
+        }
+      }
+    }
   }
 }
 
@@ -527,10 +550,9 @@
   unsigned short* qbuf = wot + (size_t)1024 * 1024;
   unsigned short* kbuf = qbuf + (size_t)8192 * 1024;
   unsigned short* vtb  = kbuf + (size_t)8192 * 256;
-  unsigned short* ao   = xb;
-
-  conv_all<<<8832, 256, 0, stream>>>(hs, Wq, Wk, Wv, Wo, xb, wqkv, wot);
-  gemm_qkv<<<192, 512, 0, stream>>>(xb, wqkv, qbuf, kbuf, vtb);
-  attn<<<512, 512, 0, stream>>>(qbuf, kbuf, vtb, ao);
-  gemm_o<<<256, 512, 0, stream>>>(ao, wot, out);
+
+  void* ka[12] = {(void*)&hs, (void*)&Wq, (void*)&Wk, (void*)&Wv, (void*)&Wo,
+                  (void*)&xb, (void*)&wqkv, (void*)&wot, (void*)&qbuf,
+                  (void*)&kbuf, (void*)&vtb, (void*)&out};
+  hipLaunchCooperativeKernel((const void*)mega, dim3(256), dim3(512), ka, 0, stream);
 }
```

Result: slower. 292.7 us (+60.9%).
